# Kernel tuning notes

Hardware: AMD Instinct MI355X
Metric: run time of the kernel (lower is better)

The kernel has to match this reference:

```python
import jax, jax.numpy as jnp
import numpy as np

MM_DIM, RANK = 1600, 15  # block.fusions.Mutan defaults
NUM_CLASSES = 95
QT_SLICES = {0: (0, 2), 1: (0, 2), 2: (2, 7), 3: (7, 95)}  # column ranges per question type

def _init(key, shape, fan_in):
    bound = 1.0 / np.sqrt(fan_in)
    return jax.random.uniform(key, shape, jnp.float32, -bound, bound)

def setup_inputs() -> dict:
    key = jax.random.key(0)
    ks = iter(jax.random.split(key, 64))
    B = 4096
    inp = {
        'input_v': jax.random.normal(next(ks), (B, 768), jnp.float32),
        'input_q': jax.random.normal(next(ks), (B, 2400), jnp.float32),
        'question_type': jax.random.randint(next(ks), (B,), 0, 4, jnp.int64),
        # projection linears
        'Wv': _init(next(ks), (1200, 768), 768), 'bv': _init(next(ks), (1200,), 768),
        'Wq': _init(next(ks), (1200, 2400), 2400), 'bq': _init(next(ks), (1200,), 2400),
        # Mutan
        'W0': _init(next(ks), (MM_DIM, 1200), 1200), 'b0': _init(next(ks), (MM_DIM,), 1200),
        'W1': _init(next(ks), (MM_DIM, 1200), 1200), 'b1': _init(next(ks), (MM_DIM,), 1200),
        'Wm0': _init(next(ks), (MM_DIM * RANK, MM_DIM), MM_DIM), 'bm0': _init(next(ks), (MM_DIM * RANK,), MM_DIM),
        'Wm1': _init(next(ks), (MM_DIM * RANK, MM_DIM), MM_DIM), 'bm1': _init(next(ks), (MM_DIM * RANK,), MM_DIM),
        'Wo': _init(next(ks), (1200, MM_DIM), MM_DIM), 'bo': _init(next(ks), (1200,), MM_DIM),
    }
    # per-question-type classifiers: 1200 -> 256 -> num_answers
    for qt, na in {0: 2, 1: 2, 2: 5, 3: 88}.items():
        inp[f'c{qt}_W1'] = _init(next(ks), (256, 1200), 1200)
        inp[f'c{qt}_b1'] = _init(next(ks), (256,), 1200)
        inp[f'c{qt}_W2'] = _init(next(ks), (na, 256), 256)
        inp[f'c{qt}_b2'] = _init(next(ks), (na,), 256)
    return inp


def reference(input_v, input_q, question_type,
              Wv, bv, Wq, bq, W0, b0, W1, b1, Wm0, bm0, Wm1, bm1, Wo, bo,
              c0_W1, c0_b1, c0_W2, c0_b2, c1_W1, c1_b1, c1_W2, c1_b2,
              c2_W1, c2_b1, c2_W2, c2_b2, c3_W1, c3_b1, c3_W2, c3_b2):
    # dropouts are identity in eval mode
    x_v = jnp.tanh(input_v @ Wv.T + bv)          # [B, 1200]
    x_q = jnp.tanh(input_q @ Wq.T + bq)          # [B, 1200]
    # Mutan fusion (mm_dim=1600, rank=15, normalize=False)
    h0 = x_v @ W0.T + b0                          # [B, 1600]
    h1 = x_q @ W1.T + b1                          # [B, 1600]
    m = (h0 @ Wm0.T + bm0) * (h1 @ Wm1.T + bm1)   # [B, 24000]
    z = m.reshape(m.shape[0], RANK, MM_DIM).sum(axis=1)  # [B, 1600]
    x = z @ Wo.T + bo                             # [B, 1200]
    # per-question-type classifiers, vectorized over full batch then masked
    cls = {0: (c0_W1, c0_b1, c0_W2, c0_b2), 1: (c1_W1, c1_b1, c1_W2, c1_b2),
           2: (c2_W1, c2_b1, c2_W2, c2_b2), 3: (c3_W1, c3_b1, c3_W2, c3_b2)}
    final = jnp.zeros((x.shape[0], NUM_CLASSES), x.dtype)
    for qt, (W1c, b1c, W2c, b2c) in cls.items():
        pred = jnp.tanh(x @ W1c.T + b1c) @ W2c.T + b2c  # [B, n_ans]
        lo, hi = QT_SLICES[qt]
        padded = jnp.pad(pred, ((0, 0), (lo, NUM_CLASSES - hi)))
        mask = (question_type == qt)[:, None]
        final = final + jnp.where(mask, padded, 0.0)
    return final
```

## Files before the change

### kernel.cpp

```cpp
#include <hip/hip_runtime.h>


using u16 = unsigned short;
typedef __bf16 b16x8 __attribute__((ext_vector_type(8)));
typedef float f32x4 __attribute__((ext_vector_type(4)));

static __device__ __forceinline__ u16 f2bf(float f) {
  unsigned int u = __builtin_bit_cast(unsigned int, f);
  u = (u + 0x7fffu + ((u >> 16) & 1u)) >> 16;
  return (u16)u;
}
static __device__ __forceinline__ float bf2f(u16 h) {
  return __builtin_bit_cast(float, (unsigned int)h << 16);
}

static __device__ __forceinline__ void gload_lds16(const u16* g, u16* l) {
  __builtin_amdgcn_global_load_lds((__attribute__((address_space(1))) void*)(g),
                                   (__attribute__((address_space(3))) void*)(l), 16, 0, 0);
}

static __device__ __forceinline__ int lds_off(int row, int slot) {
  return row * 32 + ((slot ^ ((row >> 1) & 3)) << 3);
}


__global__ void cvt_pad_kernel(const float* __restrict__ src, u16* __restrict__ dst,
                               int Ns, int Ks, int Nd, int Kd) {
  long long idx = (long long)blockIdx.x * blockDim.x + threadIdx.x;
  long long total = ((long long)Nd * Kd) >> 3;
  if (idx >= total) return;
  long long e = idx << 3;
  int r = (int)(e / Kd);
  int c = (int)(e - (long long)r * Kd);
  u16 v[8];
  if (r < Ns && c + 8 <= Ks) {
    const float* s = src + (long long)r * Ks + c;
#pragma unroll
    for (int i = 0; i < 8; ++i) v[i] = f2bf(s[i]);
  } else {
#pragma unroll
    for (int i = 0; i < 8; ++i) {
      int cc = c + i;
      float f = (r < Ns && cc < Ks) ? src[(long long)r * Ks + cc] : 0.f;
      v[i] = f2bf(f);
    }
  }
  uint4 o;
  o.x = (unsigned)v[0] | ((unsigned)v[1] << 16);
  o.y = (unsigned)v[2] | ((unsigned)v[3] << 16);
  o.z = (unsigned)v[4] | ((unsigned)v[5] << 16);
  o.w = (unsigned)v[6] | ((unsigned)v[7] << 16);
  *reinterpret_cast<uint4*>(dst + e) = o;
}

__global__ void pad_f32_kernel(const float* __restrict__ src, float* __restrict__ dst,
                               int Ns, int Nd) {
  int i = blockIdx.x * blockDim.x + threadIdx.x;
  if (i < Nd) dst[i] = (i < Ns) ? src[i] : 0.f;
}

template <int TANH, int OUT_BF16>
__global__ __launch_bounds__(256) void gemm_bt_kernel(
    const u16* __restrict__ A, const u16* __restrict__ B,
    const float* __restrict__ bias, void* __restrict__ Cv,
    int K, int Nout, int Nfill, int ldc) {
  __shared__ u16 sA[128 * 32];
  __shared__ u16 sB[128 * 32];
  const int tid = threadIdx.x;
  const int wid = tid >> 6;
  const int lane = tid & 63;
  const long long brow = (long long)blockIdx.y * 128;
  const long long bcol = (long long)blockIdx.x * 128;
  const int wr = (wid >> 1) * 64;
  const int wc = (wid & 1) * 64;
  const int lr = lane & 15;
  const int slot = lane >> 4;

  f32x4 acc[4][4];
#pragma unroll
  for (int i = 0; i < 4; ++i)
#pragma unroll
    for (int j = 0; j < 4; ++j)
#pragma unroll
      for (int q = 0; q < 4; ++q) acc[i][j][q] = 0.f;

  for (int k0 = 0; k0 < K; k0 += 32) {
    __syncthreads();
#pragma unroll
    for (int j = 0; j < 2; ++j) {
      const int c = j * 256 + tid;
      const int r = c >> 2;
      const int kc = ((c & 3) ^ ((r >> 1) & 3)) * 8;
      gload_lds16(A + (brow + r) * K + k0 + kc, sA + c * 8);
      gload_lds16(B + (bcol + r) * K + k0 + kc, sB + c * 8);
    }
    __syncthreads();
    b16x8 af[4], bfr[4];
#pragma unroll
    for (int i = 0; i < 4; ++i) {
      af[i]  = *reinterpret_cast<const b16x8*>(&sA[lds_off(wr + i * 16 + lr, slot)]);
      bfr[i] = *reinterpret_cast<const b16x8*>(&sB[lds_off(wc + i * 16 + lr, slot)]);
    }
#pragma unroll
    for (int i = 0; i < 4; ++i)
#pragma unroll
      for (int j = 0; j < 4; ++j)
        acc[i][j] = __builtin_amdgcn_mfma_f32_16x16x32_bf16(af[i], bfr[j], acc[i][j], 0, 0, 0);
  }

  const int rbase = wr + (lane >> 4) * 4;
#pragma unroll
  for (int i = 0; i < 4; ++i) {
#pragma unroll
    for (int j = 0; j < 4; ++j) {
      const long long col = bcol + wc + j * 16 + lr;
      if (col < Nfill) {
        const float bb = (col < Nout) ? bias[col] : 0.f;
#pragma unroll
        for (int q = 0; q < 4; ++q) {
          float v = acc[i][j][q] + bb;
          if (TANH) v = tanhf(v);
          if (col >= Nout) v = 0.f;
          const long long row = brow + rbase + i * 16 + q;
          if (OUT_BF16)
            reinterpret_cast<u16*>(Cv)[row * ldc + col] = f2bf(v);
          else
            reinterpret_cast<float*>(Cv)[row * ldc + col] = v;
        }
      }
    }
  }
}

template <int TANH>
__global__ __launch_bounds__(512, 2) void gemm256_dual_kernel(
    const u16* __restrict__ A0, const u16* __restrict__ Bg0,
    const float* __restrict__ bias0, u16* __restrict__ C0,
    const u16* __restrict__ A1, const u16* __restrict__ Bg1,
    const float* __restrict__ bias1, u16* __restrict__ C1,
    int K, int Nout, int ldc) {
  __shared__ u16 sAB[65536];
  const int tid = threadIdx.x;
  const int lane = tid & 63;
  const int wid = tid >> 6;
  const int wm = wid >> 2;
  const int wn = wid & 3;

  const int gy = gridDim.y;
  const int nwg = 16 * gy * gridDim.z;
  int flat = blockIdx.x + 16 * (blockIdx.y + gy * blockIdx.z);
  flat = (flat & 7) * (nwg >> 3) + (flat >> 3);
  const int m = flat & 15;
  const int rest = flat >> 4;
  const int n = rest % gy;
  const int z = rest / gy;

  const long long brow = (long long)m * 256;
  const long long bcol = (long long)n * 256;
  const u16* Ag = z ? A1 : A0;
  const u16* Bg = z ? Bg1 : Bg0;
  const float* bias = z ? bias1 : bias0;
  u16* C = z ? C1 : C0;
  const int nt = K >> 6;

  auto stage = [&](int isB, int buf, int kh, int kbase) {
    const u16* G = isB ? Bg : Ag;
    const long long rbase = isB ? bcol : brow;
    u16* ldst = &sAB[(isB ? 32768 : 0) + buf * 16384 + kh * 8192 + tid * 8];
#pragma unroll
    for (int rh = 0; rh < 2; ++rh) {
      const int row = rh * 128 + (tid >> 2);
      const int gcol = kbase + kh * 32 + (((tid & 3) ^ ((row >> 1) & 3)) << 3);
      gload_lds16(G + (rbase + row) * K + gcol, ldst + rh * 4096);
    }
  };
  auto rdA = [&](int buf, int fr, int ksub) {
    const int row = wm * 128 + fr * 16 + (lane & 15);
    return *reinterpret_cast<const b16x8*>(
        &sAB[buf * 16384 + ksub * 8192 + lds_off(row, lane >> 4)]);
  };
  auto rdB = [&](int buf, int fj, int ksub) {
    const int row = wn * 64 + fj * 16 + (lane & 15);
    return *reinterpret_cast<const b16x8*>(
        &sAB[32768 + buf * 16384 + ksub * 8192 + lds_off(row, lane >> 4)]);
  };

  f32x4 acc[8][4];
#pragma unroll
  for (int i = 0; i < 8; ++i)
#pragma unroll
    for (int j = 0; j < 4; ++j)
#pragma unroll
      for (int q = 0; q < 4; ++q) acc[i][j][q] = 0.f;

  stage(0, 0, 0, 0); stage(1, 0, 0, 0); stage(0, 0, 1, 0); stage(1, 0, 1, 0);
  stage(0, 1, 0, 64); stage(1, 1, 0, 64);
  asm volatile("s_waitcnt vmcnt(4)" ::: "memory");
  __builtin_amdgcn_s_barrier();

  b16x8 af[4], bf[4];
  for (int t = 0; t < nt; ++t) {
    const int cur = t & 1;
    const int kn1 = (t + 1) << 6, kn2 = (t + 2) << 6;
    if (t + 1 == nt) {
      asm volatile("s_waitcnt vmcnt(0)" ::: "memory");
      __builtin_amdgcn_s_barrier();
    }
#pragma unroll
    for (int j = 0; j < 4; ++j) bf[j] = rdB(cur, j, 0);
#pragma unroll
    for (int i = 0; i < 4; ++i) af[i] = rdA(cur, i, 0);
    if (t + 1 < nt) stage(0, cur ^ 1, 1, kn1);
    __builtin_amdgcn_s_barrier();
    __builtin_amdgcn_s_setprio(1);
#pragma unroll
    for (int i = 0; i < 4; ++i)
#pragma unroll
      for (int j = 0; j < 4; ++j)
        acc[i][j] = __builtin_amdgcn_mfma_f32_16x16x32_bf16(af[i], bf[j], acc[i][j], 0, 0, 0);
    __builtin_amdgcn_s_setprio(0);
    __builtin_amdgcn_s_barrier();
#pragma unroll
    for (int i = 0; i < 4; ++i) af[i] = rdA(cur, 4 + i, 0);
    if (t + 1 < nt) stage(1, cur ^ 1, 1, kn1);
    __builtin_amdgcn_s_barrier();
    __builtin_amdgcn_s_setprio(1);
#pragma unroll
    for (int i = 0; i < 4; ++i)
#pragma unroll
      for (int j = 0; j < 4; ++j)
        acc[4 + i][j] = __builtin_amdgcn_mfma_f32_16x16x32_bf16(af[i], bf[j], acc[4 + i][j], 0, 0, 0);
    __builtin_amdgcn_s_setprio(0);
    asm volatile("s_waitcnt vmcnt(8)" ::: "memory");
    __builtin_amdgcn_s_barrier();
#pragma unroll
    for (int j = 0; j < 4; ++j) bf[j] = rdB(cur, j, 1);
#pragma unroll
    for (int i = 0; i < 4; ++i) af[i] = rdA(cur, i, 1);
    if (t + 2 < nt) stage(0, cur, 0, kn2);
    __builtin_amdgcn_s_barrier();
    __builtin_amdgcn_s_setprio(1);
#pragma unroll
    for (int i = 0; i < 4; ++i)
#pragma unroll
      for (int j = 0; j < 4; ++j)
        acc[i][j] = __builtin_amdgcn_mfma_f32_16x16x32_bf16(af[i], bf[j], acc[i][j], 0, 0, 0);
    __builtin_amdgcn_s_setprio(0);
    __builtin_amdgcn_s_barrier();
#pragma unroll
    for (int i = 0; i < 4; ++i) af[i] = rdA(cur, 4 + i, 1);
    if (t + 2 < nt) stage(1, cur, 0, kn2);
    __builtin_amdgcn_s_barrier();
    __builtin_amdgcn_s_setprio(1);
#pragma unroll
    for (int i = 0; i < 4; ++i)
#pragma unroll
      for (int j = 0; j < 4; ++j)
        acc[4 + i][j] = __builtin_amdgcn_mfma_f32_16x16x32_bf16(af[i], bf[j], acc[4 + i][j], 0, 0, 0);
    __builtin_amdgcn_s_setprio(0);
    asm volatile("s_waitcnt vmcnt(8)" ::: "memory");
    __builtin_amdgcn_s_barrier();
  }

  __syncthreads();
  const long long gcb = bcol + wn * 64;
  float* lp = reinterpret_cast<float*>(sAB) + wid * 1104;
  if (gcb < Nout) {
    float bv4[4];
#pragma unroll
    for (int j = 0; j < 4; ++j) bv4[j] = bias[gcb + j * 16 + (lane & 15)];
#pragma unroll
    for (int fr = 0; fr < 8; ++fr) {
#pragma unroll
      for (int j = 0; j < 4; ++j)
#pragma unroll
        for (int q = 0; q < 4; ++q)
          lp[((lane >> 4) * 4 + q) * 68 + j * 16 + (lane & 15)] = acc[fr][j][q] + bv4[j];
#pragma unroll
      for (int p = 0; p < 2; ++p) {
        const int row = p * 8 + (lane >> 3);
        float f[8];
        *reinterpret_cast<float4*>(&f[0]) =
            *reinterpret_cast<const float4*>(&lp[row * 68 + (lane & 7) * 8]);
        *reinterpret_cast<float4*>(&f[4]) =
            *reinterpret_cast<const float4*>(&lp[row * 68 + (lane & 7) * 8 + 4]);
        uint4 o;
        if (TANH) {
#pragma unroll
          for (int k = 0; k < 8; ++k) f[k] = tanhf(f[k]);
        }
        o.x = (unsigned)f2bf(f[0]) | ((unsigned)f2bf(f[1]) << 16);
        o.y = (unsigned)f2bf(f[2]) | ((unsigned)f2bf(f[3]) << 16);
        o.z = (unsigned)f2bf(f[4]) | ((unsigned)f2bf(f[5]) << 16);
        o.w = (unsigned)f2bf(f[6]) | ((unsigned)f2bf(f[7]) << 16);
        const long long grow = brow + wm * 128 + fr * 16 + row;
        *reinterpret_cast<uint4*>(&C[grow * ldc + gcb + (lane & 7) * 8]) = o;
      }
    }
  }
}

template <int FIRST>
__global__ __launch_bounds__(256) void rank_mul_kernel(
    const u16* __restrict__ M0, const u16* __restrict__ M1,
    float* __restrict__ ZF, int rc, int ldm) {
  const int idx = blockIdx.x * 256 + threadIdx.x;
  const int b = idx / 200;
  const int d0 = (idx - b * 200) * 8;
  const u16* p0 = M0 + (long long)b * ldm + d0;
  const u16* p1 = M1 + (long long)b * ldm + d0;
  float acc[8];
#pragma unroll
  for (int i = 0; i < 8; ++i) acc[i] = 0.f;
  for (int r = 0; r < rc; ++r) {
    const uint4 a = *reinterpret_cast<const uint4*>(p0 + r * 1600);
    const uint4 c = *reinterpret_cast<const uint4*>(p1 + r * 1600);
    const unsigned aw[4] = {a.x, a.y, a.z, a.w};
    const unsigned cw[4] = {c.x, c.y, c.z, c.w};
#pragma unroll
    for (int k = 0; k < 4; ++k) {
      acc[2 * k]     += bf2f((u16)(aw[k] & 0xffff)) * bf2f((u16)(cw[k] & 0xffff));
      acc[2 * k + 1] += bf2f((u16)(aw[k] >> 16))    * bf2f((u16)(cw[k] >> 16));
    }
  }
  float* z = ZF + (long long)b * 1600 + d0;
  if (FIRST) {
#pragma unroll
    for (int i = 0; i < 8; ++i) z[i] = acc[i];
  } else {
#pragma unroll
    for (int i = 0; i < 8; ++i) z[i] += acc[i];
  }
}

__global__ __launch_bounds__(256) void head_kernel(
    const float* __restrict__ T, const int* __restrict__ qtype,
    const float* __restrict__ W20, const float* __restrict__ b20,
    const float* __restrict__ W21, const float* __restrict__ b21,
    const float* __restrict__ W22, const float* __restrict__ b22,
    const float* __restrict__ W23, const float* __restrict__ b23,
    float* __restrict__ out) {
  const int b = blockIdx.x * 4 + (threadIdx.x >> 6);
  const int lane = threadIdx.x & 63;
  const int qt = qtype[b];
  const float* W2 = (qt == 0) ? W20 : (qt == 1) ? W21 : (qt == 2) ? W22 : W23;
  const float* b2 = (qt == 0) ? b20 : (qt == 1) ? b21 : (qt == 2) ? b22 : b23;
  const int lo = (qt == 2) ? 2 : (qt == 3) ? 7 : 0;
  const int hi = (qt == 3) ? 95 : (qt == 2) ? 7 : 2;
  const float* trow = T + (long long)b * 1024 + qt * 256;
  for (int c = lane; c < 95; c += 64) {
    float v = 0.f;
    if (c >= lo && c < hi) {
      const int jj = c - lo;
      const float* w = W2 + jj * 256;
      float acc = b2[jj];
      for (int k = 0; k < 256; k += 4) {
        const float4 tv = *reinterpret_cast<const float4*>(trow + k);
        const float4 wv = *reinterpret_cast<const float4*>(w + k);
        acc += tv.x * wv.x + tv.y * wv.y + tv.z * wv.z + tv.w * wv.w;
      }
      v = acc;
    }
    out[(long long)b * 95 + c] = v;
  }
}


extern "C" void kernel_launch(void* const* d_in, const int* in_sizes, int n_in,
                              void* d_out, int out_size, void* d_ws, size_t ws_size,
                              hipStream_t stream) {
  (void)in_sizes; (void)n_in; (void)out_size; (void)ws_size;
  const float* input_v = (const float*)d_in[0];
  const float* input_q = (const float*)d_in[1];
  const int*   qtype   = (const int*)d_in[2];
  const float* Wv  = (const float*)d_in[3];  const float* bv  = (const float*)d_in[4];
  const float* Wq  = (const float*)d_in[5];  const float* bq  = (const float*)d_in[6];
  const float* W0  = (const float*)d_in[7];  const float* b0  = (const float*)d_in[8];
  const float* W1  = (const float*)d_in[9];  const float* b1  = (const float*)d_in[10];
  const float* Wm0 = (const float*)d_in[11]; const float* bm0 = (const float*)d_in[12];
  const float* Wm1 = (const float*)d_in[13]; const float* bm1 = (const float*)d_in[14];
  const float* Wo  = (const float*)d_in[15]; const float* bo  = (const float*)d_in[16];
  const float* cW1[4] = {(const float*)d_in[17], (const float*)d_in[21],
                         (const float*)d_in[25], (const float*)d_in[29]};
  const float* cb1[4] = {(const float*)d_in[18], (const float*)d_in[22],
                         (const float*)d_in[26], (const float*)d_in[30]};
  const float* cW2[4] = {(const float*)d_in[19], (const float*)d_in[23],
                         (const float*)d_in[27], (const float*)d_in[31]};
  const float* cb2[4] = {(const float*)d_in[20], (const float*)d_in[24],
                         (const float*)d_in[28], (const float*)d_in[32]};

  char* ws = (char*)d_ws;
  u16*   H0  = (u16*)(ws + 0);
  u16*   H1  = (u16*)(ws + 13107200);
  float* ZF  = (float*)(ws + 26214400);
  char*  S   = ws + 52428800;
  u16*   XV  = (u16*)(S + 0);
  u16*   XQ  = (u16*)(S + 9961472);
  char*  S3  = S + 19922944;
  u16*   WMC0 = (u16*)(S + 0);
  u16*   WMC1 = (u16*)(S + 21299200);
  u16*   M0C  = (u16*)(S + 42598400);
  u16*   M1C  = (u16*)(S + 95027200);
  u16*   ZB  = (u16*)(S + 0);
  u16*   XB  = (u16*)(S + 13107200);
  float* TB  = (float*)(S + 23068672);
  char*  S5  = S + 39845888;
  float* BVP = (float*)(ws + 210000000);
  float* BQP = (float*)(ws + 210005120);
  float* B0P = (float*)(ws + 210010240);
  float* B1P = (float*)(ws + 210016896);
  float* BOP = (float*)(ws + 210023552);
  float* B1C = (float*)(ws + 210028672);

  const dim3 blk(256);
  auto cvt = [&](const float* s, u16* d, int Ns, int Ks, int Nd, int Kd) {
    long long total = ((long long)Nd * Kd) >> 3;
    cvt_pad_kernel<<<dim3((unsigned)((total + 255) / 256)), blk, 0, stream>>>(s, d, Ns, Ks, Nd, Kd);
  };
  auto padb = [&](const float* s, float* d, int Ns, int Nd) {
    pad_f32_kernel<<<dim3((unsigned)((Nd + 255) / 256)), blk, 0, stream>>>(s, d, Ns, Nd);
  };

  padb(bv, BVP, 1200, 1280);
  padb(bq, BQP, 1200, 1280);
  padb(b0, B0P, 1600, 1664);
  padb(b1, B1P, 1600, 1664);
  padb(bo, BOP, 1200, 1280);
  for (int qt = 0; qt < 4; ++qt) padb(cb1[qt], B1C + qt * 256, 256, 256);

  {
    u16* INV = (u16*)S3;
    u16* WVB = (u16*)(S3 + 6291456);
    cvt(input_v, INV, 4096, 768, 4096, 768);
    cvt(Wv, WVB, 1200, 768, 1280, 768);
    gemm_bt_kernel<1, 1><<<dim3(10, 32), blk, 0, stream>>>(INV, WVB, BVP, XV, 768, 1200, 1216, 1216);
  }
  {
    u16* INQ = (u16*)S3;
    u16* WQB = (u16*)(S3 + 19660800);
    cvt(input_q, INQ, 4096, 2400, 4096, 2400);
    cvt(Wq, WQB, 1200, 2400, 1280, 2400);
    gemm_bt_kernel<1, 1><<<dim3(10, 32), blk, 0, stream>>>(INQ, WQB, BQP, XQ, 2400, 1200, 1216, 1216);
  }
  {
    u16* W0B = (u16*)S3;
    u16* W1B = (u16*)(S3 + 4358144);
    cvt(W0, W0B, 1600, 1200, 1792, 1216);
    cvt(W1, W1B, 1600, 1200, 1792, 1216);
    gemm256_dual_kernel<0><<<dim3(16, 7, 2), dim3(512), 0, stream>>>(
        XV, W0B, B0P, H0, XQ, W1B, B1P, H1, 1216, 1600, 1600);
  }
  for (int c = 0; c < 4; ++c) {
    const int rc = (c < 3) ? 4 : 3;
    const int cols = rc * 1600;
    const int NB = (cols + 255) / 256;
    const int rowsPad = NB * 256;
    const long long roff = (long long)c * 6400;
    cvt(Wm0 + roff * 1600, WMC0, cols, 1600, rowsPad, 1600);
    cvt(Wm1 + roff * 1600, WMC1, cols, 1600, rowsPad, 1600);
    gemm256_dual_kernel<0><<<dim3(16, NB, 2), dim3(512), 0, stream>>>(
        H0, WMC0, bm0 + roff, M0C, H1, WMC1, bm1 + roff, M1C, 1600, cols, cols);
    if (c == 0)
      rank_mul_kernel<1><<<dim3(3200), blk, 0, stream>>>(M0C, M1C, ZF, rc, cols);
    else
      rank_mul_kernel<0><<<dim3(3200), blk, 0, stream>>>(M0C, M1C, ZF, rc, cols);
  }
  cvt(ZF, ZB, 4096, 1600, 4096, 1600);
  {
    u16* WOB = (u16*)S5;
    cvt(Wo, WOB, 1200, 1600, 1280, 1600);
    gemm_bt_kernel<0, 1><<<dim3(10, 32), blk, 0, stream>>>(ZB, WOB, BOP, XB, 1600, 1200, 1216, 1216);
  }
  {
    u16* CW1B = (u16*)S5;
    for (int qt = 0; qt < 4; ++qt)
      cvt(cW1[qt], CW1B + (long long)qt * 256 * 1216, 256, 1200, 256, 1216);
    gemm_bt_kernel<1, 0><<<dim3(8, 32), blk, 0, stream>>>(XB, CW1B, B1C, TB, 1216, 1024, 1024, 1024);
  }
  head_kernel<<<dim3(1024), blk, 0, stream>>>(TB, qtype,
      cW2[0], cb2[0], cW2[1], cb2[1], cW2[2], cb2[2], cW2[3], cb2[3],
      (float*)d_out);
}
```

Baseline: 1.255 ms.

## Merge bias pads into one launch, fuse Z bf16 convert, unroll GEMM loop

The nine small bias-padding launches are merged into one batched kernel that takes a job table. The last rank_mul pass now writes the bf16 Z directly, which removes a separate fp32-to-bf16 conversion kernel and its extra read and write of Z. The 256-tile dual GEMM main loop is rewritten with macros: it unrolls two iterations, uses precomputed incrementing global pointers and LDS bases, and peels the tail instead of testing branches every iteration. The gains are lower launch overhead, less memory traffic and less address arithmetic, at the cost of more macro-heavy code.

```diff
diff --git a/kernel.cpp b/kernel.cpp
--- a/kernel.cpp
+++ b/kernel.cpp
@@ -53,10 +53,16 @@
   *reinterpret_cast<uint4*>(dst + e) = o;
 }
 
-__global__ void pad_f32_kernel(const float* __restrict__ src, float* __restrict__ dst,
-                               int Ns, int Nd) {
-  int i = blockIdx.x * blockDim.x + threadIdx.x;
-  if (i < Nd) dst[i] = (i < Ns) ? src[i] : 0.f;
+struct PadJobs {
+  const float* s[9];
+  float* d[9];
+  int ns[9];
+  int nd[9];
+};
+__global__ __launch_bounds__(256) void pad_all_kernel(PadJobs pj) {
+  const int job = blockIdx.y;
+  const int i = blockIdx.x * 256 + threadIdx.x;
+  if (i < pj.nd[job]) pj.d[job][i] = (i < pj.ns[job]) ? pj.s[job][i] : 0.f;
 }
 
 template <int TANH, int OUT_BF16>
@@ -163,27 +169,83 @@
   u16* C = z ? C1 : C0;
   const int nt = K >> 6;
 
-  auto stage = [&](int isB, int buf, int kh, int kbase) {
-    const u16* G = isB ? Bg : Ag;
-    const long long rbase = isB ? bcol : brow;
-    u16* ldst = &sAB[(isB ? 32768 : 0) + buf * 16384 + kh * 8192 + tid * 8];
-#pragma unroll
-    for (int rh = 0; rh < 2; ++rh) {
-      const int row = rh * 128 + (tid >> 2);
-      const int gcol = kbase + kh * 32 + (((tid & 3) ^ ((row >> 1) & 3)) << 3);
-      gload_lds16(G + (rbase + row) * K + gcol, ldst + rh * 4096);
-    }
-  };
-  auto rdA = [&](int buf, int fr, int ksub) {
-    const int row = wm * 128 + fr * 16 + (lane & 15);
-    return *reinterpret_cast<const b16x8*>(
-        &sAB[buf * 16384 + ksub * 8192 + lds_off(row, lane >> 4)]);
-  };
-  auto rdB = [&](int buf, int fj, int ksub) {
-    const int row = wn * 64 + fj * 16 + (lane & 15);
-    return *reinterpret_cast<const b16x8*>(
-        &sAB[32768 + buf * 16384 + ksub * 8192 + lds_off(row, lane >> 4)]);
-  };
+  const int srow = tid >> 2;
+  const int scol = ((tid & 3) ^ ((srow >> 1) & 3)) << 3;
+  const u16* pA  = Ag + (brow + srow) * K + scol;
+  const u16* pA2 = pA + (long long)128 * K;
+  const u16* pB  = Bg + (bcol + srow) * K + scol;
+  const u16* pB2 = pB + (long long)128 * K;
+
+  const int lr = lane & 15;
+  const int slot = lane >> 4;
+  const int aRow = wm * 128 + lr;
+  const int aBase = aRow * 32 + ((slot ^ ((aRow >> 1) & 3)) << 3);
+  const int bRow = wn * 64 + lr;
+  const int bBase = bRow * 32 + ((slot ^ ((bRow >> 1) & 3)) << 3);
+
+#define STAGE_A(LOFF)                                        \
+  do {                                                       \
+    gload_lds16(pA, &sAB[(LOFF) + tid * 8]);                 \
+    gload_lds16(pA2, &sAB[(LOFF) + 4096 + tid * 8]);         \
+    pA += 32; pA2 += 32;                                     \
+  } while (0)
+#define STAGE_B(LOFF)                                        \
+  do {                                                       \
+    gload_lds16(pB, &sAB[32768 + (LOFF) + tid * 8]);         \
+    gload_lds16(pB2, &sAB[32768 + (LOFF) + 4096 + tid * 8]); \
+    pB += 32; pB2 += 32;                                     \
+  } while (0)
+#define RD_A(BUF, FR, KS) \
+  (*reinterpret_cast<const b16x8*>(&sAB[(BUF) * 16384 + (KS) * 8192 + aBase + (FR) * 512]))
+#define RD_B(BUF, FJ, KS) \
+  (*reinterpret_cast<const b16x8*>(&sAB[32768 + (BUF) * 16384 + (KS) * 8192 + bBase + (FJ) * 512]))
+#define MFMA16(R)                                                            \
+  do {                                                                       \
+    acc[(R)+0][0] = __builtin_amdgcn_mfma_f32_16x16x32_bf16(af[0], bfr[0], acc[(R)+0][0], 0, 0, 0); \
+    acc[(R)+0][1] = __builtin_amdgcn_mfma_f32_16x16x32_bf16(af[0], bfr[1], acc[(R)+0][1], 0, 0, 0); \
+    acc[(R)+0][2] = __builtin_amdgcn_mfma_f32_16x16x32_bf16(af[0], bfr[2], acc[(R)+0][2], 0, 0, 0); \
+    acc[(R)+0][3] = __builtin_amdgcn_mfma_f32_16x16x32_bf16(af[0], bfr[3], acc[(R)+0][3], 0, 0, 0); \
+    acc[(R)+1][0] = __builtin_amdgcn_mfma_f32_16x16x32_bf16(af[1], bfr[0], acc[(R)+1][0], 0, 0, 0); \
+    acc[(R)+1][1] = __builtin_amdgcn_mfma_f32_16x16x32_bf16(af[1], bfr[1], acc[(R)+1][1], 0, 0, 0); \
+    acc[(R)+1][2] = __builtin_amdgcn_mfma_f32_16x16x32_bf16(af[1], bfr[2], acc[(R)+1][2], 0, 0, 0); \
+    acc[(R)+1][3] = __builtin_amdgcn_mfma_f32_16x16x32_bf16(af[1], bfr[3], acc[(R)+1][3], 0, 0, 0); \
+    acc[(R)+2][0] = __builtin_amdgcn_mfma_f32_16x16x32_bf16(af[2], bfr[0], acc[(R)+2][0], 0, 0, 0); \
+    acc[(R)+2][1] = __builtin_amdgcn_mfma_f32_16x16x32_bf16(af[2], bfr[1], acc[(R)+2][1], 0, 0, 0); \
+    acc[(R)+2][2] = __builtin_amdgcn_mfma_f32_16x16x32_bf16(af[2], bfr[2], acc[(R)+2][2], 0, 0, 0); \
+    acc[(R)+2][3] = __builtin_amdgcn_mfma_f32_16x16x32_bf16(af[2], bfr[3], acc[(R)+2][3], 0, 0, 0); \
+    acc[(R)+3][0] = __builtin_amdgcn_mfma_f32_16x16x32_bf16(af[3], bfr[0], acc[(R)+3][0], 0, 0, 0); \
+    acc[(R)+3][1] = __builtin_amdgcn_mfma_f32_16x16x32_bf16(af[3], bfr[1], acc[(R)+3][1], 0, 0, 0); \
+    acc[(R)+3][2] = __builtin_amdgcn_mfma_f32_16x16x32_bf16(af[3], bfr[2], acc[(R)+3][2], 0, 0, 0); \
+    acc[(R)+3][3] = __builtin_amdgcn_mfma_f32_16x16x32_bf16(af[3], bfr[3], acc[(R)+3][3], 0, 0, 0); \
+  } while (0)
+#define VM8 asm volatile("s_waitcnt vmcnt(8)" ::: "memory")
+#define VM0 asm volatile("s_waitcnt vmcnt(0)" ::: "memory")
+#define BAR __builtin_amdgcn_s_barrier()
+#define PRIO1 __builtin_amdgcn_s_setprio(1)
+#define PRIO0 __builtin_amdgcn_s_setprio(0)
+#define BODY(BUF, G1, G2)                                               \
+  do {                                                                  \
+    bfr[0] = RD_B(BUF, 0, 0); bfr[1] = RD_B(BUF, 1, 0);                 \
+    bfr[2] = RD_B(BUF, 2, 0); bfr[3] = RD_B(BUF, 3, 0);                 \
+    af[0] = RD_A(BUF, 0, 0); af[1] = RD_A(BUF, 1, 0);                   \
+    af[2] = RD_A(BUF, 2, 0); af[3] = RD_A(BUF, 3, 0);                   \
+    if (G1) STAGE_A((BUF ^ 1) * 16384 + 8192);                          \
+    BAR; PRIO1; MFMA16(0); PRIO0; BAR;                                  \
+    af[0] = RD_A(BUF, 4, 0); af[1] = RD_A(BUF, 5, 0);                   \
+    af[2] = RD_A(BUF, 6, 0); af[3] = RD_A(BUF, 7, 0);                   \
+    if (G1) STAGE_B((BUF ^ 1) * 16384 + 8192);                          \
+    BAR; PRIO1; MFMA16(4); PRIO0; VM8; BAR;                             \
+    bfr[0] = RD_B(BUF, 0, 1); bfr[1] = RD_B(BUF, 1, 1);                 \
+    bfr[2] = RD_B(BUF, 2, 1); bfr[3] = RD_B(BUF, 3, 1);                 \
+    af[0] = RD_A(BUF, 0, 1); af[1] = RD_A(BUF, 1, 1);                   \
+    af[2] = RD_A(BUF, 2, 1); af[3] = RD_A(BUF, 3, 1);                   \
+    if (G2) STAGE_A((BUF) * 16384);                                     \
+    BAR; PRIO1; MFMA16(0); PRIO0; BAR;                                  \
+    af[0] = RD_A(BUF, 4, 1); af[1] = RD_A(BUF, 5, 1);                   \
+    af[2] = RD_A(BUF, 6, 1); af[3] = RD_A(BUF, 7, 1);                   \
+    if (G2) STAGE_B((BUF) * 16384);                                     \
+    BAR; PRIO1; MFMA16(4); PRIO0; VM8; BAR;                             \
+  } while (0)
 
   f32x4 acc[8][4];
 #pragma unroll
@@ -193,74 +255,37 @@
 #pragma unroll
       for (int q = 0; q < 4; ++q) acc[i][j][q] = 0.f;
 
-  stage(0, 0, 0, 0); stage(1, 0, 0, 0); stage(0, 0, 1, 0); stage(1, 0, 1, 0);
-  stage(0, 1, 0, 64); stage(1, 1, 0, 64);
+  STAGE_A(0); STAGE_B(0);
+  STAGE_A(8192); STAGE_B(8192);
+  STAGE_A(16384); STAGE_B(16384);
   asm volatile("s_waitcnt vmcnt(4)" ::: "memory");
-  __builtin_amdgcn_s_barrier();
-
-  b16x8 af[4], bf[4];
-  for (int t = 0; t < nt; ++t) {
-    const int cur = t & 1;
-    const int kn1 = (t + 1) << 6, kn2 = (t + 2) << 6;
-    if (t + 1 == nt) {
-      asm volatile("s_waitcnt vmcnt(0)" ::: "memory");
-      __builtin_amdgcn_s_barrier();
-    }
-#pragma unroll
-    for (int j = 0; j < 4; ++j) bf[j] = rdB(cur, j, 0);
-#pragma unroll
-    for (int i = 0; i < 4; ++i) af[i] = rdA(cur, i, 0);
-    if (t + 1 < nt) stage(0, cur ^ 1, 1, kn1);
-    __builtin_amdgcn_s_barrier();
-    __builtin_amdgcn_s_setprio(1);
-#pragma unroll
-    for (int i = 0; i < 4; ++i)
-#pragma unroll
-      for (int j = 0; j < 4; ++j)
-        acc[i][j] = __builtin_amdgcn_mfma_f32_16x16x32_bf16(af[i], bf[j], acc[i][j], 0, 0, 0);
-    __builtin_amdgcn_s_setprio(0);
-    __builtin_amdgcn_s_barrier();
-#pragma unroll
-    for (int i = 0; i < 4; ++i) af[i] = rdA(cur, 4 + i, 0);
-    if (t + 1 < nt) stage(1, cur ^ 1, 1, kn1);
-    __builtin_amdgcn_s_barrier();
-    __builtin_amdgcn_s_setprio(1);
-#pragma unroll
-    for (int i = 0; i < 4; ++i)
-#pragma unroll
-      for (int j = 0; j < 4; ++j)
-        acc[4 + i][j] = __builtin_amdgcn_mfma_f32_16x16x32_bf16(af[i], bf[j], acc[4 + i][j], 0, 0, 0);
-    __builtin_amdgcn_s_setprio(0);
-    asm volatile("s_waitcnt vmcnt(8)" ::: "memory");
-    __builtin_amdgcn_s_barrier();
-#pragma unroll
-    for (int j = 0; j < 4; ++j) bf[j] = rdB(cur, j, 1);
-#pragma unroll
-    for (int i = 0; i < 4; ++i) af[i] = rdA(cur, i, 1);
-    if (t + 2 < nt) stage(0, cur, 0, kn2);
-    __builtin_amdgcn_s_barrier();
-    __builtin_amdgcn_s_setprio(1);
-#pragma unroll
-    for (int i = 0; i < 4; ++i)
-#pragma unroll
-      for (int j = 0; j < 4; ++j)
-        acc[i][j] = __builtin_amdgcn_mfma_f32_16x16x32_bf16(af[i], bf[j], acc[i][j], 0, 0, 0);
-    __builtin_amdgcn_s_setprio(0);
-    __builtin_amdgcn_s_barrier();
-#pragma unroll
-    for (int i = 0; i < 4; ++i) af[i] = rdA(cur, 4 + i, 1);
-    if (t + 2 < nt) stage(1, cur, 0, kn2);
-    __builtin_amdgcn_s_barrier();
-    __builtin_amdgcn_s_setprio(1);
-#pragma unroll
-    for (int i = 0; i < 4; ++i)
-#pragma unroll
-      for (int j = 0; j < 4; ++j)
-        acc[4 + i][j] = __builtin_amdgcn_mfma_f32_16x16x32_bf16(af[i], bf[j], acc[4 + i][j], 0, 0, 0);
-    __builtin_amdgcn_s_setprio(0);
-    asm volatile("s_waitcnt vmcnt(8)" ::: "memory");
-    __builtin_amdgcn_s_barrier();
-  }
+  BAR;
+
+  b16x8 af[4], bfr[4];
+  int t = 0;
+  for (; t + 2 < nt; t += 2) {
+    BODY(0, true, true);
+    BODY(1, true, (t + 3 < nt));
+  }
+  if (nt & 1) {
+    VM0; BAR;
+    BODY(0, false, false);
+  } else {
+    BODY(0, true, false);
+    VM0; BAR;
+    BODY(1, false, false);
+  }
+#undef BODY
+#undef STAGE_A
+#undef STAGE_B
+#undef RD_A
+#undef RD_B
+#undef MFMA16
+#undef VM8
+#undef VM0
+#undef BAR
+#undef PRIO1
+#undef PRIO0
 
   __syncthreads();
   const long long gcb = bcol + wn * 64;
@@ -268,14 +293,14 @@
   if (gcb < Nout) {
     float bv4[4];
 #pragma unroll
-    for (int j = 0; j < 4; ++j) bv4[j] = bias[gcb + j * 16 + (lane & 15)];
+    for (int j = 0; j < 4; ++j) bv4[j] = bias[gcb + j * 16 + lr];
 #pragma unroll
     for (int fr = 0; fr < 8; ++fr) {
 #pragma unroll
       for (int j = 0; j < 4; ++j)
 #pragma unroll
         for (int q = 0; q < 4; ++q)
-          lp[((lane >> 4) * 4 + q) * 68 + j * 16 + (lane & 15)] = acc[fr][j][q] + bv4[j];
+          lp[(slot * 4 + q) * 68 + j * 16 + lr] = acc[fr][j][q] + bv4[j];
 #pragma unroll
       for (int p = 0; p < 2; ++p) {
         const int row = p * 8 + (lane >> 3);
@@ -284,11 +309,11 @@
             *reinterpret_cast<const float4*>(&lp[row * 68 + (lane & 7) * 8]);
         *reinterpret_cast<float4*>(&f[4]) =
             *reinterpret_cast<const float4*>(&lp[row * 68 + (lane & 7) * 8 + 4]);
-        uint4 o;
         if (TANH) {
 #pragma unroll
           for (int k = 0; k < 8; ++k) f[k] = tanhf(f[k]);
         }
+        uint4 o;
         o.x = (unsigned)f2bf(f[0]) | ((unsigned)f2bf(f[1]) << 16);
         o.y = (unsigned)f2bf(f[2]) | ((unsigned)f2bf(f[3]) << 16);
         o.z = (unsigned)f2bf(f[4]) | ((unsigned)f2bf(f[5]) << 16);
@@ -300,10 +325,10 @@
   }
 }
 
-template <int FIRST>
+template <int FIRST, int EMITB>
 __global__ __launch_bounds__(256) void rank_mul_kernel(
     const u16* __restrict__ M0, const u16* __restrict__ M1,
-    float* __restrict__ ZF, int rc, int ldm) {
+    float* __restrict__ ZF, u16* __restrict__ ZB, int rc, int ldm) {
   const int idx = blockIdx.x * 256 + threadIdx.x;
   const int b = idx / 200;
   const int d0 = (idx - b * 200) * 8;
@@ -323,13 +348,22 @@
       acc[2 * k + 1] += bf2f((u16)(aw[k] >> 16))    * bf2f((u16)(cw[k] >> 16));
     }
   }
-  float* z = ZF + (long long)b * 1600 + d0;
-  if (FIRST) {
-#pragma unroll
-    for (int i = 0; i < 8; ++i) z[i] = acc[i];
+  float* zf = ZF + (long long)b * 1600 + d0;
+  if (EMITB) {
+#pragma unroll
+    for (int i = 0; i < 8; ++i) acc[i] += zf[i];
+    uint4 o;
+    o.x = (unsigned)f2bf(acc[0]) | ((unsigned)f2bf(acc[1]) << 16);
+    o.y = (unsigned)f2bf(acc[2]) | ((unsigned)f2bf(acc[3]) << 16);
+    o.z = (unsigned)f2bf(acc[4]) | ((unsigned)f2bf(acc[5]) << 16);
+    o.w = (unsigned)f2bf(acc[6]) | ((unsigned)f2bf(acc[7]) << 16);
+    *reinterpret_cast<uint4*>(ZB + (long long)b * 1600 + d0) = o;
+  } else if (FIRST) {
+#pragma unroll
+    for (int i = 0; i < 8; ++i) zf[i] = acc[i];
   } else {
 #pragma unroll
-    for (int i = 0; i < 8; ++i) z[i] += acc[i];
+    for (int i = 0; i < 8; ++i) zf[i] += acc[i];
   }
 }
 
@@ -417,16 +451,16 @@
     long long total = ((long long)Nd * Kd) >> 3;
     cvt_pad_kernel<<<dim3((unsigned)((total + 255) / 256)), blk, 0, stream>>>(s, d, Ns, Ks, Nd, Kd);
   };
-  auto padb = [&](const float* s, float* d, int Ns, int Nd) {
-    pad_f32_kernel<<<dim3((unsigned)((Nd + 255) / 256)), blk, 0, stream>>>(s, d, Ns, Nd);
-  };
-
-  padb(bv, BVP, 1200, 1280);
-  padb(bq, BQP, 1200, 1280);
-  padb(b0, B0P, 1600, 1664);
-  padb(b1, B1P, 1600, 1664);
-  padb(bo, BOP, 1200, 1280);
-  for (int qt = 0; qt < 4; ++qt) padb(cb1[qt], B1C + qt * 256, 256, 256);
+
+  {
+    PadJobs pj;
+    const float* ss[9] = {bv, bq, b0, b1, bo, cb1[0], cb1[1], cb1[2], cb1[3]};
+    float* dd[9] = {BVP, BQP, B0P, B1P, BOP, B1C, B1C + 256, B1C + 512, B1C + 768};
+    int nss[9] = {1200, 1200, 1600, 1600, 1200, 256, 256, 256, 256};
+    int ndd[9] = {1280, 1280, 1664, 1664, 1280, 256, 256, 256, 256};
+    for (int i = 0; i < 9; ++i) { pj.s[i] = ss[i]; pj.d[i] = dd[i]; pj.ns[i] = nss[i]; pj.nd[i] = ndd[i]; }
+    pad_all_kernel<<<dim3(7, 9), blk, 0, stream>>>(pj);
+  }
 
   {
     u16* INV = (u16*)S3;
@@ -461,11 +495,12 @@
     gemm256_dual_kernel<0><<<dim3(16, NB, 2), dim3(512), 0, stream>>>(
         H0, WMC0, bm0 + roff, M0C, H1, WMC1, bm1 + roff, M1C, 1600, cols, cols);
     if (c == 0)
-      rank_mul_kernel<1><<<dim3(3200), blk, 0, stream>>>(M0C, M1C, ZF, rc, cols);
+      rank_mul_kernel<1, 0><<<dim3(3200), blk, 0, stream>>>(M0C, M1C, ZF, ZB, rc, cols);
+    else if (c < 3)
+      rank_mul_kernel<0, 0><<<dim3(3200), blk, 0, stream>>>(M0C, M1C, ZF, ZB, rc, cols);
     else
-      rank_mul_kernel<0><<<dim3(3200), blk, 0, stream>>>(M0C, M1C, ZF, rc, cols);
-  }
-  cvt(ZF, ZB, 4096, 1600, 4096, 1600);
+      rank_mul_kernel<0, 1><<<dim3(3200), blk, 0, stream>>>(M0C, M1C, ZF, ZB, rc, cols);
+  }
   {
     u16* WOB = (u16*)S5;
     cvt(Wo, WOB, 1200, 1600, 1280, 1600);
```

New measurement: 2.497 ms. 1.99x slower.
